# Optimization experiments

Hardware: AMD Instinct MI355X
Metric: run time of the kernel (lower is better)

The kernel has to match this reference:

```python
import jax, jax.numpy as jnp
import numpy as np

B, U, N0, N1, E, H = 8, 8192, 64, 64, 128, 8
S = N0 * N1


def setup_inputs() -> dict:
    key = jax.random.key(0)
    ks = jax.random.split(key, 9)
    # regular grid over [-1, 1]^2 (meshgrid, 'ij' indexing)
    c0 = jnp.linspace(-1.0, 1.0, N0)
    c1 = jnp.linspace(-1.0, 1.0, N1)
    g0, g1 = jnp.meshgrid(c0, c1, indexing='ij')
    xc_on_grid = jnp.broadcast_to(jnp.stack([g0, g1], -1), (B, N0, N1, 2))
    xc_off_grid = jax.random.uniform(ks[0], (B, U, 2), minval=-1.0, maxval=1.0)
    zc_off_grid = jax.random.normal(ks[1], (B, U, E))
    zc_on_grid = jax.random.normal(ks[2], (B, N0, N1, E))
    latents = jax.random.normal(ks[3], (N0, N1, E))
    fake_embedding = jax.random.normal(ks[4], (E,))
    sc = 1.0 / np.sqrt(E).astype(np.float32)
    Wq = jax.random.normal(ks[5], (E, E)) * sc
    Wk = jax.random.normal(ks[6], (E, E)) * sc
    Wv = jax.random.normal(ks[7], (E, E)) * sc
    Wo = jax.random.normal(ks[8], (E, E)) * sc
    return dict(xc_off_grid=xc_off_grid, xc_on_grid=xc_on_grid,
                zc_off_grid=zc_off_grid, zc_on_grid=zc_on_grid,
                latents=latents, fake_embedding=fake_embedding,
                Wq=Wq, Wk=Wk, Wv=Wv, Wo=Wo, used_modality=0)


def _nearest_idx(x, x_grid):
    # nearest cell on a regular grid, flattened row-major (k=1 of nearest_gridded_neighbours)
    n0, n1 = x_grid.shape[1], x_grid.shape[2]
    c0 = x_grid[:, :, 0, 0]   # [B, n0]
    c1 = x_grid[:, 0, :, 1]   # [B, n1]
    sp0 = (c0[:, 1] - c0[:, 0])[:, None]
    sp1 = (c1[:, 1] - c1[:, 0])[:, None]
    i0 = jnp.clip(jnp.round((x[..., 0] - c0[:, :1]) / sp0), 0, n0 - 1)
    i1 = jnp.clip(jnp.round((x[..., 1] - c1[:, :1]) / sp1), 0, n1 - 1)
    return (i0 * n1 + i1).astype(jnp.int32)


def _cumcount(nearest):
    # duplicate-count within each grid cell via linear-recurrence associative scan
    # (same math as the torch complex-log scan: x_t = a_t*x_{t-1} + b_t, a=b=same-flag)
    sort_idx = jnp.argsort(nearest, axis=1, stable=True)
    ns = jnp.take_along_axis(nearest, sort_idx, axis=1)
    same = (ns == jnp.roll(ns, 1, axis=1)).astype(jnp.float32)
    same = same.at[:, 0].set(0.0)

    def combine(c1, c2):
        a1, b1 = c1
        a2, b2 = c2
        return a1 * a2, a2 * b1 + b2

    _, cc = jax.lax.associative_scan(combine, (same, same), axis=1)
    unsort = jnp.argsort(sort_idx, axis=1, stable=True)
    return jnp.take_along_axis(jnp.round(cc), unsort, axis=1).astype(jnp.int32)


def _mhca(q, kv, mask, Wq, Wk, Wv, Wo):
    # q: [N,1,E], kv: [N,P,E], mask: [N,1,P] (True = attend)
    N, P, Ed = kv.shape
    dh = Ed // H
    qh = (q @ Wq).reshape(N, 1, H, dh).transpose(0, 2, 1, 3)
    kh = (kv @ Wk).reshape(N, P, H, dh).transpose(0, 2, 1, 3)
    vh = (kv @ Wv).reshape(N, P, H, dh).transpose(0, 2, 1, 3)
    scores = jnp.einsum('nhqd,nhkd->nhqk', qh, kh) / jnp.sqrt(jnp.asarray(dh, qh.dtype))
    scores = jnp.where(mask[:, None, :, :], scores, -jnp.inf)
    attn = jax.nn.softmax(scores, axis=-1)
    out = jnp.einsum('nhqk,nhkd->nhqd', attn, vh)
    return out.transpose(0, 2, 1, 3).reshape(N, 1, Ed) @ Wo


def reference(xc_off_grid, xc_on_grid, zc_off_grid, zc_on_grid, latents,
              fake_embedding, Wq, Wk, Wv, Wo, used_modality):
    # PseudoTokenGridEncoder.forward, no-coarsening branch, used_modality=OFF_GRID
    Bb, Uu, Ee = zc_off_grid.shape
    n0, n1 = xc_on_grid.shape[1], xc_on_grid.shape[2]
    Ss = n0 * n1
    nearest = _nearest_idx(xc_off_grid, xc_on_grid)         # [B, U]
    cumcount = _cumcount(nearest)                           # [B, U]
    max_patch = int(jnp.max(cumcount)) + 2                  # data-dependent (eager)
    rows = nearest.reshape(-1) + jnp.repeat(jnp.arange(Bb) * Ss, Uu)
    cols = cumcount.reshape(-1)
    grid_stacked = jnp.zeros((Bb * Ss, max_patch, Ee), zc_off_grid.dtype)
    grid_stacked = grid_stacked.at[rows, cols].set(zc_off_grid.reshape(Bb * Uu, Ee))
    grid_stacked = grid_stacked.at[:, -1].set(fake_embedding)  # OFF_GRID -> fake token
    valid = jnp.zeros((Bb * Ss, max_patch), bool)
    valid = valid.at[rows, cols].set(True).at[:, -1].set(True)
    latent_flat = jnp.broadcast_to(latents.reshape(1, Ss, Ee), (Bb, Ss, Ee)).reshape(Bb * Ss, 1, Ee)
    out = _mhca(latent_flat, grid_stacked, valid[:, None, :], Wq, Wk, Wv, Wo)
    z_grid = out.reshape(Bb, n0, n1, Ee)
    return xc_on_grid, z_grid
```

## Files before the change

### kernel.cpp

```cpp
#include <hip/hip_runtime.h>
#include <hip/hip_bf16.h>

#define NB 8
#define NU 8192
#define GN0 64
#define GN1 64
#define NS 4096
#define NE 128
#define NH 8
#define CAP 20
#define NPTS (NB * NU)
#define NCELL (NB * NS)
#define OUT0 (NB * GN0 * GN1 * 2)


typedef __attribute__((ext_vector_type(8))) short short8v;
typedef __attribute__((ext_vector_type(4))) float float4v;

static __device__ inline unsigned pk2(float a, float b) {
  __hip_bfloat16 x = __float2bfloat16(a), y = __float2bfloat16(b);
  return ((unsigned)*(unsigned short*)&y << 16) | *(unsigned short*)&x;
}
static __device__ inline float bfs(short v) {
  unsigned u = (unsigned)(unsigned short)v << 16;
  return __builtin_bit_cast(float, u);
}

__global__ __launch_bounds__(256) void setup_kernel(
    const float* __restrict__ xc_on, const float* __restrict__ fake,
    const float* __restrict__ latents,
    const float* __restrict__ Wq, const float* __restrict__ Wk,
    const float* __restrict__ Wv, const float* __restrict__ Wo,
    float* __restrict__ out, int* __restrict__ counts,
    float* __restrict__ fakeKV, __hip_bfloat16* __restrict__ Wt,
    __hip_bfloat16* __restrict__ Wot, float* __restrict__ qf) {
  int t = threadIdx.x;
  int blk = blockIdx.x;
  if (blk < 256) {
    int i = blk * 256 + t;
    out[i] = xc_on[i];
    if (i < NCELL) counts[i] = 0;
    return;
  }
  if (blk == 256) {
    __shared__ float frow[NE];
    if (t < NE) frow[t] = fake[t];
    __syncthreads();
    int e = t & 127, half = t >> 7;
    const float* W = half ? Wv : Wk;
    float acc = 0.f;
    for (int j = 0; j < NE; ++j) acc += frow[j] * W[j * NE + e];
    fakeKV[half * NE + e] = acc;
    return;
  }
  if (blk <= 320) {
    int flat = (blk - 257) * 256 + t;
    int j = flat >> 7, e = flat & 127;
    Wt[e * NE + j] = __float2bfloat16(Wv[flat]);
    Wt[(128 + e) * NE + j] = __float2bfloat16(Wk[flat]);
    Wot[e * NE + j] = __float2bfloat16(Wo[flat]);
    return;
  }
  int s0 = (blk - 321) * 8;
  __shared__ float lrow[8][NE];
  for (int i = t; i < 8 * NE; i += 256)
    lrow[i >> 7][i & 127] = latents[(size_t)s0 * NE + i];
  __syncthreads();
  for (int i = t; i < 8 * NE; i += 256) {
    int sl = i >> 7, e = i & 127;
    float acc = 0.f;
    for (int j = 0; j < NE; ++j) acc += lrow[sl][j] * Wq[j * NE + e];
    qf[(size_t)(s0 + sl) * NE + e] = acc;
  }
}

__global__ __launch_bounds__(256) void vgemm_kernel(
    const float* __restrict__ z, const float* __restrict__ xc_off,
    const float* __restrict__ xc_on, const __hip_bfloat16* __restrict__ Wt,
    int* __restrict__ counts, unsigned short* __restrict__ lists,
    __hip_bfloat16* __restrict__ Vb, __hip_bfloat16* __restrict__ Kb) {
  __shared__ __hip_bfloat16 zb[64 * 136];
  int tid = threadIdx.x;
  size_t row0 = (size_t)blockIdx.x * 64;
  for (int n = 0; n < 8; ++n) {
    int flat = n * 1024 + tid * 4;
    int r = flat >> 7, c = flat & 127;
    float4 v = *(const float4*)&z[(row0 + r) * NE + c];
    uint2 u = {pk2(v.x, v.y), pk2(v.z, v.w)};
    *(uint2*)&zb[r * 136 + c] = u;
  }
  if (tid < 64) {
    int p = (int)row0 + tid;
    int b = p >> 13;
    const float* g = xc_on + (size_t)b * (GN0 * GN1 * 2);
    float c00 = g[0], c01 = g[GN1 * 2], c10 = g[1], c11 = g[3];
    float x0 = xc_off[(size_t)p * 2 + 0];
    float x1 = xc_off[(size_t)p * 2 + 1];
    float f0 = rintf((x0 - c00) / (c01 - c00));
    float f1 = rintf((x1 - c10) / (c11 - c10));
    int i0 = (int)fminf(fmaxf(f0, 0.f), 63.f);
    int i1 = (int)fminf(fmaxf(f1, 0.f), 63.f);
    int cell = b * NS + i0 * GN1 + i1;
    int pos = atomicAdd(&counts[cell], 1);
    if (pos < CAP) lists[cell * CAP + pos] = (unsigned short)p;
  }
  __syncthreads();
  int wid = tid >> 6, l = tid & 63;
  int lr = l & 15, lk = l >> 4;
  const short* zl = (const short*)zb;
  const short* Wg = (const short*)Wt;
  float4v acc[4][4] = {};
  short8v bfrag[4][4];
#pragma unroll
  for (int ct = 0; ct < 4; ++ct) {
    int col = wid * 64 + ct * 16 + lr;
#pragma unroll
    for (int ks = 0; ks < 4; ++ks)
      bfrag[ct][ks] = *(const short8v*)&Wg[col * NE + ks * 32 + lk * 8];
  }
#pragma unroll
  for (int ks = 0; ks < 4; ++ks)
#pragma unroll
    for (int st = 0; st < 4; ++st) {
      short8v a = *(const short8v*)&zl[(st * 16 + lr) * 136 + ks * 32 + lk * 8];
#pragma unroll
      for (int ct = 0; ct < 4; ++ct)
        acc[st][ct] = __builtin_amdgcn_mfma_f32_16x16x32_bf16(a, bfrag[ct][ks], acc[st][ct], 0, 0, 0);
    }
  __hip_bfloat16* dst = (wid < 2) ? Vb : Kb;
  int cb = (wid & 1) * 64;
#pragma unroll
  for (int st = 0; st < 4; ++st)
#pragma unroll
    for (int ct = 0; ct < 4; ++ct)
#pragma unroll
      for (int r = 0; r < 4; ++r) {
        size_t row = row0 + st * 16 + lk * 4 + r;
        int col = cb + ct * 16 + lr;
        dst[row * NE + col] = __float2bfloat16(acc[st][ct][r]);
      }
}

__global__ __launch_bounds__(256) void attn_wo_kernel(
    const __hip_bfloat16* __restrict__ Vb, const __hip_bfloat16* __restrict__ Kb,
    const float* __restrict__ qf, const float* __restrict__ fakeKV,
    const int* __restrict__ counts, const unsigned short* __restrict__ lists,
    const __hip_bfloat16* __restrict__ Wot, float* __restrict__ out) {
  __shared__ __hip_bfloat16 ob[16 * 136];
  __shared__ float sc[4][24][8];
  int tid = threadIdx.x, w = tid >> 6, l = tid & 63;
  int cell0 = blockIdx.x * 16;
  for (int ci = 0; ci < 4; ++ci) {
    int row = w * 4 + ci;
    int cell = cell0 + row;
    int s = cell & (NS - 1);
    int cnt = min(counts[cell], CAP);
    float2 qv = *(const float2*)&qf[(size_t)s * NE + 2 * l];
    int mypid = (l < cnt) ? (int)lists[cell * CAP + l] : 0;
    for (int t = 0; t < cnt; ++t) {
      int pid = __shfl(mypid, t);
      unsigned kd = ((const unsigned*)(Kb + (size_t)pid * NE))[l];
      float p = qv.x * bfs((short)(kd & 0xffff)) + qv.y * bfs((short)(kd >> 16));
      p += __shfl_xor(p, 1); p += __shfl_xor(p, 2); p += __shfl_xor(p, 4);
      if ((l & 7) == 0) sc[w][t][l >> 3] = p * 0.25f;
    }
    {
      float2 fk = *(const float2*)&fakeKV[2 * l];
      float p = qv.x * fk.x + qv.y * fk.y;
      p += __shfl_xor(p, 1); p += __shfl_xor(p, 2); p += __shfl_xor(p, 4);
      if ((l & 7) == 0) sc[w][cnt][l >> 3] = p * 0.25f;
    }
    __builtin_amdgcn_wave_barrier();
    if (l < 8) {
      int T = cnt + 1;
      float m = -1e30f;
      for (int t = 0; t < T; ++t) m = fmaxf(m, sc[w][t][l]);
      float sum = 0.f;
      for (int t = 0; t < T; ++t) {
        float e = __expf(sc[w][t][l] - m);
        sum += e;
        sc[w][t][l] = e;
      }
      float inv = 1.f / sum;
      for (int t = 0; t < T; ++t) sc[w][t][l] *= inv;
    }
    __builtin_amdgcn_wave_barrier();
    int h = l >> 3;
    float acc0 = 0.f, acc1 = 0.f;
    for (int t = 0; t < cnt; ++t) {
      int pid = __shfl(mypid, t);
      unsigned vv = ((const unsigned*)(Vb + (size_t)pid * NE))[l];
      float wt = sc[w][t][h];
      acc0 += wt * bfs((short)(vv & 0xffff));
      acc1 += wt * bfs((short)(vv >> 16));
    }
    float2 fv = *(const float2*)&fakeKV[NE + 2 * l];
    float wt = sc[w][cnt][h];
    acc0 += wt * fv.x;
    acc1 += wt * fv.y;
    *(unsigned*)&ob[row * 136 + 2 * l] = pk2(acc0, acc1);
  }
  __syncthreads();
  int lr = l & 15, lk = l >> 4;
  const short* ol = (const short*)ob;
  const short* Wg = (const short*)Wot;
  short8v afr[4];
#pragma unroll
  for (int ks = 0; ks < 4; ++ks)
    afr[ks] = *(const short8v*)&ol[lr * 136 + ks * 32 + lk * 8];
  float4v acc[2] = {};
#pragma unroll
  for (int ct = 0; ct < 2; ++ct) {
    int col = (w * 2 + ct) * 16 + lr;
#pragma unroll
    for (int ks = 0; ks < 4; ++ks) {
      short8v bfr = *(const short8v*)&Wg[col * NE + ks * 32 + lk * 8];
      acc[ct] = __builtin_amdgcn_mfma_f32_16x16x32_bf16(afr[ks], bfr, acc[ct], 0, 0, 0);
    }
  }
  float* base = out + (size_t)OUT0 + (size_t)blockIdx.x * 16 * NE;
#pragma unroll
  for (int ct = 0; ct < 2; ++ct)
#pragma unroll
    for (int r = 0; r < 4; ++r) {
      int row = lk * 4 + r;
      int col = (w * 2 + ct) * 16 + lr;
      base[(size_t)row * NE + col] = acc[ct][r];
    }
}

extern "C" void kernel_launch(void* const* d_in, const int* in_sizes, int n_in,
                              void* d_out, int out_size, void* d_ws, size_t ws_size,
                              hipStream_t stream) {
  const float* xc_off  = (const float*)d_in[0];
  const float* xc_on   = (const float*)d_in[1];
  const float* zc_off  = (const float*)d_in[2];
  const float* latents = (const float*)d_in[4];
  const float* fake    = (const float*)d_in[5];
  const float* Wq      = (const float*)d_in[6];
  const float* Wk      = (const float*)d_in[7];
  const float* Wv      = (const float*)d_in[8];
  const float* Wo      = (const float*)d_in[9];
  float* out = (float*)d_out;

  char* ws = (char*)d_ws;
  int*            counts = (int*)(ws);
  unsigned short* lists  = (unsigned short*)(ws + 131072);
  float*          qf     = (float*)(ws + 1441792);
  float*          fakeKV = (float*)(ws + 3538944);
  __hip_bfloat16* Wt     = (__hip_bfloat16*)(ws + 3539968);
  __hip_bfloat16* Wot    = (__hip_bfloat16*)(ws + 3605504);
  __hip_bfloat16* Vb     = (__hip_bfloat16*)(ws + 3638272);
  __hip_bfloat16* Kb     = (__hip_bfloat16*)(ws + 20415488);

  hipLaunchKernelGGL(setup_kernel, dim3(833), dim3(256), 0, stream,
                     xc_on, fake, latents, Wq, Wk, Wv, Wo,
                     out, counts, fakeKV, Wt, Wot, qf);
  hipLaunchKernelGGL(vgemm_kernel, dim3(NPTS / 64), dim3(256), 0, stream,
                     zc_off, xc_off, xc_on, Wt, counts, lists, Vb, Kb);
  hipLaunchKernelGGL(attn_wo_kernel, dim3(NCELL / 16), dim3(256), 0, stream,
                     Vb, Kb, qf, fakeKV, counts, lists, Wot, out);
}
```

Baseline: 69.70 us.

## Process four cells per wave in parallel and swizzle block order

Result: faster. 59.51 us (-14.6%).

```diff
diff --git a/kernel.cpp b/kernel.cpp
--- a/kernel.cpp
+++ b/kernel.cpp
@@ -81,7 +81,8 @@
     __hip_bfloat16* __restrict__ Vb, __hip_bfloat16* __restrict__ Kb) {
   __shared__ __hip_bfloat16 zb[64 * 136];
   int tid = threadIdx.x;
-  size_t row0 = (size_t)blockIdx.x * 64;
+  int blk = ((int)blockIdx.x & 7) * 128 + ((int)blockIdx.x >> 3);
+  size_t row0 = (size_t)blk * 64;
   for (int n = 0; n < 8; ++n) {
     int flat = n * 1024 + tid * 4;
     int r = flat >> 7, c = flat & 127;
@@ -147,58 +148,72 @@
     const int* __restrict__ counts, const unsigned short* __restrict__ lists,
     const __hip_bfloat16* __restrict__ Wot, float* __restrict__ out) {
   __shared__ __hip_bfloat16 ob[16 * 136];
-  __shared__ float sc[4][24][8];
+  __shared__ float sc[4][4][24][8];
+  __shared__ unsigned short pl[4][4][24];
   int tid = threadIdx.x, w = tid >> 6, l = tid & 63;
-  int cell0 = blockIdx.x * 16;
-  for (int ci = 0; ci < 4; ++ci) {
-    int row = w * 4 + ci;
-    int cell = cell0 + row;
-    int s = cell & (NS - 1);
-    int cnt = min(counts[cell], CAP);
-    float2 qv = *(const float2*)&qf[(size_t)s * NE + 2 * l];
-    int mypid = (l < cnt) ? (int)lists[cell * CAP + l] : 0;
-    for (int t = 0; t < cnt; ++t) {
-      int pid = __shfl(mypid, t);
-      unsigned kd = ((const unsigned*)(Kb + (size_t)pid * NE))[l];
-      float p = qv.x * bfs((short)(kd & 0xffff)) + qv.y * bfs((short)(kd >> 16));
-      p += __shfl_xor(p, 1); p += __shfl_xor(p, 2); p += __shfl_xor(p, 4);
-      if ((l & 7) == 0) sc[w][t][l >> 3] = p * 0.25f;
-    }
-    {
-      float2 fk = *(const float2*)&fakeKV[2 * l];
-      float p = qv.x * fk.x + qv.y * fk.y;
-      p += __shfl_xor(p, 1); p += __shfl_xor(p, 2); p += __shfl_xor(p, 4);
-      if ((l & 7) == 0) sc[w][cnt][l >> 3] = p * 0.25f;
-    }
-    __builtin_amdgcn_wave_barrier();
-    if (l < 8) {
-      int T = cnt + 1;
-      float m = -1e30f;
-      for (int t = 0; t < T; ++t) m = fmaxf(m, sc[w][t][l]);
-      float sum = 0.f;
-      for (int t = 0; t < T; ++t) {
-        float e = __expf(sc[w][t][l] - m);
-        sum += e;
-        sc[w][t][l] = e;
-      }
-      float inv = 1.f / sum;
-      for (int t = 0; t < T; ++t) sc[w][t][l] *= inv;
-    }
-    __builtin_amdgcn_wave_barrier();
-    int h = l >> 3;
-    float acc0 = 0.f, acc1 = 0.f;
-    for (int t = 0; t < cnt; ++t) {
-      int pid = __shfl(mypid, t);
-      unsigned vv = ((const unsigned*)(Vb + (size_t)pid * NE))[l];
-      float wt = sc[w][t][h];
-      acc0 += wt * bfs((short)(vv & 0xffff));
-      acc1 += wt * bfs((short)(vv >> 16));
-    }
-    float2 fv = *(const float2*)&fakeKV[NE + 2 * l];
-    float wt = sc[w][cnt][h];
-    acc0 += wt * fv.x;
-    acc1 += wt * fv.y;
-    *(unsigned*)&ob[row * 136 + 2 * l] = pk2(acc0, acc1);
+  int g = l >> 4, i = l & 15;
+  int blk = ((int)blockIdx.x & 7) * 256 + ((int)blockIdx.x >> 3);
+  int row = w * 4 + g;
+  int cell = blk * 16 + row;
+  int s = cell & (NS - 1);
+  int cnt = min(counts[cell], CAP);
+  for (int t = i; t < cnt; t += 16)
+    pl[w][g][t] = lists[cell * CAP + t];
+  int d0 = i * 8;
+  float4 qa = *(const float4*)&qf[(size_t)s * NE + d0];
+  float4 qb = *(const float4*)&qf[(size_t)s * NE + d0 + 4];
+  __builtin_amdgcn_wave_barrier();
+  for (int t = 0; t < cnt; ++t) {
+    int pid = pl[w][g][t];
+    short8v kv = *(const short8v*)(const short*)(Kb + (size_t)pid * NE + d0);
+    float p = qa.x * bfs(kv[0]) + qa.y * bfs(kv[1]) + qa.z * bfs(kv[2]) + qa.w * bfs(kv[3])
+            + qb.x * bfs(kv[4]) + qb.y * bfs(kv[5]) + qb.z * bfs(kv[6]) + qb.w * bfs(kv[7]);
+    p += __shfl_xor(p, 1);
+    if ((i & 1) == 0) sc[w][g][t][i >> 1] = p * 0.25f;
+  }
+  {
+    float4 fa = *(const float4*)&fakeKV[d0];
+    float4 fb = *(const float4*)&fakeKV[d0 + 4];
+    float p = qa.x * fa.x + qa.y * fa.y + qa.z * fa.z + qa.w * fa.w
+            + qb.x * fb.x + qb.y * fb.y + qb.z * fb.z + qb.w * fb.w;
+    p += __shfl_xor(p, 1);
+    if ((i & 1) == 0) sc[w][g][cnt][i >> 1] = p * 0.25f;
+  }
+  __builtin_amdgcn_wave_barrier();
+  if (i < 8) {
+    int T = cnt + 1;
+    float m = -1e30f;
+    for (int t = 0; t < T; ++t) m = fmaxf(m, sc[w][g][t][i]);
+    float sum = 0.f;
+    for (int t = 0; t < T; ++t) {
+      float e = __expf(sc[w][g][t][i] - m);
+      sum += e;
+      sc[w][g][t][i] = e;
+    }
+    float inv = 1.f / sum;
+    for (int t = 0; t < T; ++t) sc[w][g][t][i] *= inv;
+  }
+  __builtin_amdgcn_wave_barrier();
+  int h = i >> 1;
+  float va[8] = {0.f, 0.f, 0.f, 0.f, 0.f, 0.f, 0.f, 0.f};
+  for (int t = 0; t < cnt; ++t) {
+    int pid = pl[w][g][t];
+    short8v vv = *(const short8v*)(const short*)(Vb + (size_t)pid * NE + d0);
+    float wt = sc[w][g][t][h];
+#pragma unroll
+    for (int j = 0; j < 8; ++j) va[j] += wt * bfs(vv[j]);
+  }
+  {
+    float4 fa = *(const float4*)&fakeKV[NE + d0];
+    float4 fb = *(const float4*)&fakeKV[NE + d0 + 4];
+    float wt = sc[w][g][cnt][h];
+    va[0] += wt * fa.x; va[1] += wt * fa.y; va[2] += wt * fa.z; va[3] += wt * fa.w;
+    va[4] += wt * fb.x; va[5] += wt * fb.y; va[6] += wt * fb.z; va[7] += wt * fb.w;
+  }
+  {
+    uint4 u = {pk2(va[0], va[1]), pk2(va[2], va[3]),
+               pk2(va[4], va[5]), pk2(va[6], va[7])};
+    *(uint4*)&ob[row * 136 + d0] = u;
   }
   __syncthreads();
   int lr = l & 15, lk = l >> 4;
@@ -218,14 +233,14 @@
       acc[ct] = __builtin_amdgcn_mfma_f32_16x16x32_bf16(afr[ks], bfr, acc[ct], 0, 0, 0);
     }
   }
-  float* base = out + (size_t)OUT0 + (size_t)blockIdx.x * 16 * NE;
+  float* base = out + (size_t)OUT0 + (size_t)blk * 16 * NE;
 #pragma unroll
   for (int ct = 0; ct < 2; ++ct)
 #pragma unroll
     for (int r = 0; r < 4; ++r) {
-      int row = lk * 4 + r;
+      int orow = lk * 4 + r;
       int col = (w * 2 + ct) * 16 + lr;
-      base[(size_t)row * NE + col] = acc[ct][r];
+      base[(size_t)orow * NE + col] = acc[ct][r];
     }
 }
 
```
